# Kernel tuning notes

Hardware: AMD Instinct MI355X
Metric: run time of the kernel (lower is better)

## Reference

```python
import jax, jax.numpy as jnp
import numpy as np

RADIUS = 0.1
MAX_NEIGHBORS = 64


def setup_inputs() -> dict:
    key0 = jax.random.key(0)
    k1, k2 = jax.random.split(key0)
    query = jax.random.uniform(k1, (4, 2048, 3), dtype=jnp.float32)
    key = jax.random.uniform(k2, (4, 8192, 3), dtype=jnp.float32)
    return {"query": query, "key": key}


def reference(query, key):
    # PointNet++-style ball query: for each query point, the indices of the
    # first MAX_NEIGHBORS key points (in key order) with squared distance
    # < RADIUS^2; remaining slots are padded with the first found neighbor
    # index (0 if no neighbor exists, matching zero-initialized CUDA output).
    B, N1, _ = query.shape
    N2 = key.shape[1]
    K = MAX_NEIGHBORS

    # [B, N1, N2] squared pairwise distances
    d2 = jnp.sum((query[:, :, None, :] - key[:, None, :, :]) ** 2, axis=-1)
    within = d2 < jnp.float32(RADIUS) ** 2  # [B, N1, N2] bool

    # slot each valid neighbor lands in (in key-index order)
    pos = jnp.cumsum(within.astype(jnp.int32), axis=-1) - 1  # [B, N1, N2]
    take = within & (pos < K)
    slot = jnp.where(take, pos, K)  # invalid entries routed to dummy slot K

    n2_idx = jnp.broadcast_to(jnp.arange(N2, dtype=jnp.int32), (B, N1, N2))
    b_idx = jnp.arange(B)[:, None, None]
    n1_idx = jnp.arange(N1)[None, :, None]

    out = jnp.full((B, N1, K + 1), -1, dtype=jnp.int32)
    # slots < K are unique per (b, n1); duplicates only at dummy slot K
    out = out.at[b_idx, n1_idx, slot].set(n2_idx)
    out = out[..., :K]  # drop dummy slot

    # pad empty slots with index of first in-radius neighbor (0 if none)
    first = jnp.argmax(within, axis=-1).astype(jnp.int32)  # [B, N1]
    out = jnp.where(out < 0, first[..., None], out)
    return out
```

## Files before the change

kernel.cpp:

```cpp
#include <hip/hip_runtime.h>


constexpr int   K    = 64;
constexpr float R2   = 0.01f;
constexpr int   B    = 4;
constexpr int   N1   = 2048;
constexpr int   N2   = 8192;
constexpr int   GC   = 5;
constexpr int   NCELL = GC * GC * GC;
constexpr float INVCELL = 5.0f;
constexpr int   SUBS_PER_B = 32;
constexpr int   SUBS       = B * SUBS_PER_B;

constexpr size_t SORTED_BYTES = (size_t)B * N2 * 16;
constexpr size_t CS_BYTES     = (size_t)B * (NCELL + 1) * 4;
constexpr size_t WS_NEEDED    = SORTED_BYTES + CS_BYTES;

__device__ __forceinline__ int cell_of(float v) {
    int c = (int)(v * INVCELL);
    return c < 0 ? 0 : (c > GC - 1 ? GC - 1 : c);
}

__global__ __launch_bounds__(256) void build_kernel(
    const float* __restrict__ key,
    int* __restrict__ cell_start,
    float4* __restrict__ sorted)
{
    __shared__ int h_tot[NCELL];
    __shared__ int h_pre[NCELL];
    __shared__ int sbuf[128];
    __shared__ int cursor[NCELL];

    const int k = blockIdx.x;
    const int b = k >> 5;
    const int s = k & 31;
    const int t = threadIdx.x;

    if (t < NCELL) { h_tot[t] = 0; h_pre[t] = 0; }
    __syncthreads();

    const float* kb = key + (size_t)b * N2 * 3;
    float mx = 0.f, my = 0.f, mz = 0.f;
    int mycell = 0;
    for (int i = 0; i < SUBS_PER_B; ++i) {
        const int j = i * 256 + t;
        const float x = kb[j * 3 + 0];
        const float y = kb[j * 3 + 1];
        const float z = kb[j * 3 + 2];
        const int c = (cell_of(x) * GC + cell_of(y)) * GC + cell_of(z);
        atomicAdd(&h_tot[c], 1);
        if (i < s) atomicAdd(&h_pre[c], 1);
        if (i == s) { mx = x; my = y; mz = z; mycell = c; }
    }
    __syncthreads();

    const int total = (t < NCELL) ? h_tot[t] : 0;
    if (t < 128) sbuf[t] = total;
    __syncthreads();
    for (int off = 1; off < 128; off <<= 1) {
        int v = 0;
        if (t < 128 && t >= off) v = sbuf[t - off];
        __syncthreads();
        if (t < 128) sbuf[t] += v;
        __syncthreads();
    }
    if (t < NCELL) {
        const int excl = sbuf[t] - total;
        cursor[t] = excl + h_pre[t];
        if (s == 0) {
            cell_start[b * (NCELL + 1) + t + 1] = sbuf[t];
            if (t == 0) cell_start[b * (NCELL + 1)] = 0;
        }
    }
    __syncthreads();

    const int pos = atomicAdd(&cursor[mycell], 1);
    float4 v;
    v.x = mx; v.y = my; v.z = mz; v.w = __int_as_float(s * 256 + t);
    sorted[(size_t)b * N2 + pos] = v;
}

__global__ __launch_bounds__(256) void ballquery_grid_kernel(
    const float* __restrict__ query,
    const float4* __restrict__ sorted,
    const int* __restrict__ cell_start,
    int* __restrict__ out)
{
    __shared__ unsigned int bm[4 * 256];

    const int lane = threadIdx.x & 63;
    const int wv   = threadIdx.x >> 6;
    const int q    = blockIdx.x * 4 + wv;
    const int b    = q >> 11;

    const float qx = query[q * 3 + 0];
    const float qy = query[q * 3 + 1];
    const float qz = query[q * 3 + 2];

    const float ux = qx * INVCELL, uy = qy * INVCELL, uz = qz * INVCELL;
    const int cx = cell_of(qx), cy = cell_of(qy), cz = cell_of(qz);
    const int nx = (ux - cx < 0.5f) ? cx - 1 : cx + 1;
    const int ny = (uy - cy < 0.5f) ? cy - 1 : cy + 1;
    const int nz = (uz - cz < 0.5f) ? cz - 1 : cz + 1;
    const int xlo = max(0, min(cx, nx)), xhi = min(GC - 1, max(cx, nx));
    const int ylo = max(0, min(cy, ny)), yhi = min(GC - 1, max(cy, ny));
    const int zlo = max(0, min(cz, nz)), zhi = min(GC - 1, max(cz, nz));

    unsigned int* wbm = bm + wv * 256;
    uint4 zz; zz.x = zz.y = zz.z = zz.w = 0u;
    ((uint4*)wbm)[lane] = zz;

    const int*    cs = cell_start + b * (NCELL + 1);
    const float4* sb = sorted + (size_t)b * N2;

    for (int xx = xlo; xx <= xhi; ++xx) {
        for (int yy = ylo; yy <= yhi; ++yy) {
            const int colz = (xx * GC + yy) * GC;
            const int s = cs[colz + zlo];
            const int e = cs[colz + zhi + 1];
            for (int t0 = s; t0 < e; t0 += 64) {
                const int i = t0 + lane;
                const float4 kv = sb[min(i, e - 1)];
                const float dx = kv.x - qx;
                const float dy = kv.y - qy;
                const float dz = kv.z - qz;
                const bool within = (i < e) && (dx * dx + dy * dy + dz * dz < R2);
                if (within) {
                    const int id = __float_as_int(kv.w);
                    atomicOr(&wbm[id >> 5], 1u << (id & 31));
                }
            }
        }
    }

    const uint4 w = ((const uint4*)wbm)[lane];
    const int c = __popc(w.x) + __popc(w.y) + __popc(w.z) + __popc(w.w);

    int x = c;
    #pragma unroll
    for (int off = 1; off < 64; off <<= 1) {
        int y = __shfl_up(x, off);
        if (lane >= off) x += y;
    }
    const int base = x - c;
    const int cnt  = __shfl(x, 63);

    int fs;
    if      (w.x) fs = __builtin_ctz(w.x);
    else if (w.y) fs = 32 + __builtin_ctz(w.y);
    else if (w.z) fs = 64 + __builtin_ctz(w.z);
    else if (w.w) fs = 96 + __builtin_ctz(w.w);
    else          fs = 0;
    int myfirst = c ? (lane << 7) + fs : 0x7fffffff;
    #pragma unroll
    for (int off = 32; off; off >>= 1)
        myfirst = min(myfirst, __shfl_xor(myfirst, off));
    const int firstIdx = (cnt == 0) ? 0 : myfirst;

    int* op = out + q * K;
    int slot = base;
    unsigned int wr[4] = {w.x, w.y, w.z, w.w};
    #pragma unroll
    for (int r = 0; r < 4; ++r) {
        unsigned int m = wr[r];
        const int bb = (lane << 7) + (r << 5);
        while (m) {
            const int bp = __builtin_ctz(m);
            m &= m - 1;
            if (slot < K) op[slot] = bb + bp;
            ++slot;
        }
    }

    const int kpad = cnt < K ? cnt : K;
    const int s2 = kpad + lane;
    if (s2 < K) op[s2] = firstIdx;
}

__global__ __launch_bounds__(256) void ballquery_bruteforce_kernel(
    const float* __restrict__ query, const float* __restrict__ key,
    int* __restrict__ out)
{
    const int lane = threadIdx.x & 63;
    const int q = blockIdx.x * 4 + (threadIdx.x >> 6);
    const int b = q >> 11;
    const float qx = query[q * 3], qy = query[q * 3 + 1], qz = query[q * 3 + 2];
    const float* kb = key + (size_t)b * N2 * 3;
    int* op = out + (size_t)q * K;
    int count = 0, first = 0;
    bool have_first = false;
    const unsigned long long lane_mask_lt = (lane == 0) ? 0ull : (~0ull >> (64 - lane));
    for (int c = 0; c < N2 / 64; ++c) {
        if (count >= K) break;
        const int j = (c << 6) + lane;
        const float* kp = kb + j * 3;
        const float dx = kp[0] - qx, dy = kp[1] - qy, dz = kp[2] - qz;
        const bool within = dx * dx + dy * dy + dz * dz < R2;
        const unsigned long long mask = __ballot(within);
        if (mask) {
            if (!have_first) { first = (c << 6) + __builtin_ctzll(mask); have_first = true; }
            if (within) {
                const int slot = count + __popcll(mask & lane_mask_lt);
                if (slot < K) op[slot] = j;
            }
            count += __popcll(mask);
        }
    }
    const int cnt = count < K ? count : K;
    if (cnt + lane < K) op[cnt + lane] = first;
}

extern "C" void kernel_launch(void* const* d_in, const int* in_sizes, int n_in,
                              void* d_out, int out_size, void* d_ws, size_t ws_size,
                              hipStream_t stream) {
    const float* query = (const float*)d_in[0];
    const float* key   = (const float*)d_in[1];
    int* out = (int*)d_out;

    if (ws_size < WS_NEEDED) {
        ballquery_bruteforce_kernel<<<(B * N1) / 4, 256, 0, stream>>>(query, key, out);
        return;
    }

    float4* sorted     = (float4*)d_ws;
    int*    cell_start = (int*)((char*)d_ws + SORTED_BYTES);

    build_kernel<<<SUBS, 256, 0, stream>>>(key, cell_start, sorted);
    ballquery_grid_kernel<<<(B * N1) / 4, 256, 0, stream>>>(query, sorted, cell_start, out);
}
```

Measured before the change: 76.09 us.

## Build cell grid with one 1024-thread block per batch; pair queries in brute-force

The grid build now runs one 1024-thread block per batch. Each thread holds 8 keys in registers, builds a single histogram and scatters its keys, replacing 32 blocks per batch that each re-read all keys to compute prefix counts. This cuts redundant global reads and atomics but leaves only 4 blocks on the GPU, so the build is less parallel. The brute-force fallback now handles two queries per wave to reuse key loads, and drops the early exit once 64 neighbors are found. That fallback only runs when the workspace is too small.

Result: faster. 72.50 us (-4.7%).

```diff
diff --git a/kernel.cpp b/kernel.cpp
--- a/kernel.cpp
+++ b/kernel.cpp
@@ -9,8 +9,7 @@
 constexpr int   GC   = 5;
 constexpr int   NCELL = GC * GC * GC;
 constexpr float INVCELL = 5.0f;
-constexpr int   SUBS_PER_B = 32;
-constexpr int   SUBS       = B * SUBS_PER_B;
+constexpr int   KPT  = N2 / 1024;
 
 constexpr size_t SORTED_BYTES = (size_t)B * N2 * 16;
 constexpr size_t CS_BYTES     = (size_t)B * (NCELL + 1) * 4;
@@ -21,40 +20,36 @@
     return c < 0 ? 0 : (c > GC - 1 ? GC - 1 : c);
 }
 
-__global__ __launch_bounds__(256) void build_kernel(
+__global__ __launch_bounds__(1024) void build_kernel(
     const float* __restrict__ key,
     int* __restrict__ cell_start,
     float4* __restrict__ sorted)
 {
-    __shared__ int h_tot[NCELL];
-    __shared__ int h_pre[NCELL];
+    __shared__ int h[NCELL];
     __shared__ int sbuf[128];
     __shared__ int cursor[NCELL];
 
-    const int k = blockIdx.x;
-    const int b = k >> 5;
-    const int s = k & 31;
+    const int b = blockIdx.x;
     const int t = threadIdx.x;
 
-    if (t < NCELL) { h_tot[t] = 0; h_pre[t] = 0; }
+    if (t < NCELL) h[t] = 0;
     __syncthreads();
 
     const float* kb = key + (size_t)b * N2 * 3;
-    float mx = 0.f, my = 0.f, mz = 0.f;
-    int mycell = 0;
-    for (int i = 0; i < SUBS_PER_B; ++i) {
-        const int j = i * 256 + t;
-        const float x = kb[j * 3 + 0];
-        const float y = kb[j * 3 + 1];
-        const float z = kb[j * 3 + 2];
-        const int c = (cell_of(x) * GC + cell_of(y)) * GC + cell_of(z);
-        atomicAdd(&h_tot[c], 1);
-        if (i < s) atomicAdd(&h_pre[c], 1);
-        if (i == s) { mx = x; my = y; mz = z; mycell = c; }
-    }
-    __syncthreads();
-
-    const int total = (t < NCELL) ? h_tot[t] : 0;
+    float kx[KPT], ky[KPT], kz[KPT];
+    int   kc[KPT];
+    #pragma unroll
+    for (int i = 0; i < KPT; ++i) {
+        const int j = i * 1024 + t;
+        kx[i] = kb[j * 3 + 0];
+        ky[i] = kb[j * 3 + 1];
+        kz[i] = kb[j * 3 + 2];
+        kc[i] = (cell_of(kx[i]) * GC + cell_of(ky[i])) * GC + cell_of(kz[i]);
+        atomicAdd(&h[kc[i]], 1);
+    }
+    __syncthreads();
+
+    const int total = (t < NCELL) ? h[t] : 0;
     if (t < 128) sbuf[t] = total;
     __syncthreads();
     for (int off = 1; off < 128; off <<= 1) {
@@ -65,19 +60,21 @@
         __syncthreads();
     }
     if (t < NCELL) {
-        const int excl = sbuf[t] - total;
-        cursor[t] = excl + h_pre[t];
-        if (s == 0) {
-            cell_start[b * (NCELL + 1) + t + 1] = sbuf[t];
-            if (t == 0) cell_start[b * (NCELL + 1)] = 0;
-        }
-    }
-    __syncthreads();
-
-    const int pos = atomicAdd(&cursor[mycell], 1);
-    float4 v;
-    v.x = mx; v.y = my; v.z = mz; v.w = __int_as_float(s * 256 + t);
-    sorted[(size_t)b * N2 + pos] = v;
+        cursor[t] = sbuf[t] - total;
+        cell_start[b * (NCELL + 1) + t + 1] = sbuf[t];
+        if (t == 0) cell_start[b * (NCELL + 1)] = 0;
+    }
+    __syncthreads();
+
+    float4* sb = sorted + (size_t)b * N2;
+    #pragma unroll
+    for (int i = 0; i < KPT; ++i) {
+        const int pos = atomicAdd(&cursor[kc[i]], 1);
+        float4 v;
+        v.x = kx[i]; v.y = ky[i]; v.z = kz[i];
+        v.w = __int_as_float(i * 1024 + t);
+        sb[pos] = v;
+    }
 }
 
 __global__ __launch_bounds__(256) void ballquery_grid_kernel(
@@ -177,37 +174,66 @@
     if (s2 < K) op[s2] = firstIdx;
 }
 
-__global__ __launch_bounds__(256) void ballquery_bruteforce_kernel(
+__global__ __launch_bounds__(256) void bq_brute2_kernel(
     const float* __restrict__ query, const float* __restrict__ key,
     int* __restrict__ out)
 {
     const int lane = threadIdx.x & 63;
-    const int q = blockIdx.x * 4 + (threadIdx.x >> 6);
-    const int b = q >> 11;
-    const float qx = query[q * 3], qy = query[q * 3 + 1], qz = query[q * 3 + 2];
+    const int w    = blockIdx.x * 4 + (threadIdx.x >> 6);
+    const int q0   = w * 2;
+    const int q1   = q0 + 1;
+    const int b    = q0 >> 11;
+
+    const float qx0 = query[q0 * 3 + 0], qy0 = query[q0 * 3 + 1], qz0 = query[q0 * 3 + 2];
+    const float qx1 = query[q1 * 3 + 0], qy1 = query[q1 * 3 + 1], qz1 = query[q1 * 3 + 2];
+
     const float* kb = key + (size_t)b * N2 * 3;
-    int* op = out + (size_t)q * K;
-    int count = 0, first = 0;
-    bool have_first = false;
-    const unsigned long long lane_mask_lt = (lane == 0) ? 0ull : (~0ull >> (64 - lane));
+    const unsigned long long below = (lane == 0) ? 0ull : (~0ull >> (64 - lane));
+
+    int cnt0 = 0, cnt1 = 0, f0 = -1, f1 = -1;
+    int* op0 = out + (size_t)q0 * K;
+    int* op1 = out + (size_t)q1 * K;
+
+    #pragma unroll 4
     for (int c = 0; c < N2 / 64; ++c) {
-        if (count >= K) break;
         const int j = (c << 6) + lane;
-        const float* kp = kb + j * 3;
-        const float dx = kp[0] - qx, dy = kp[1] - qy, dz = kp[2] - qz;
-        const bool within = dx * dx + dy * dy + dz * dz < R2;
-        const unsigned long long mask = __ballot(within);
-        if (mask) {
-            if (!have_first) { first = (c << 6) + __builtin_ctzll(mask); have_first = true; }
-            if (within) {
-                const int slot = count + __popcll(mask & lane_mask_lt);
-                if (slot < K) op[slot] = j;
+        const float x = kb[j * 3 + 0];
+        const float y = kb[j * 3 + 1];
+        const float z = kb[j * 3 + 2];
+        {
+            const float dx = x - qx0, dy = y - qy0, dz = z - qz0;
+            const bool within = dx * dx + dy * dy + dz * dz < R2;
+            const unsigned long long m = __ballot(within);
+            if (m) {
+                if (f0 < 0) f0 = (c << 6) + __builtin_ctzll(m);
+                if (within) {
+                    const int slot = cnt0 + __popcll(m & below);
+                    if (slot < K) op0[slot] = j;
+                }
+                cnt0 += __popcll(m);
             }
-            count += __popcll(mask);
-        }
-    }
-    const int cnt = count < K ? count : K;
-    if (cnt + lane < K) op[cnt + lane] = first;
+        }
+        {
+            const float dx = x - qx1, dy = y - qy1, dz = z - qz1;
+            const bool within = dx * dx + dy * dy + dz * dz < R2;
+            const unsigned long long m = __ballot(within);
+            if (m) {
+                if (f1 < 0) f1 = (c << 6) + __builtin_ctzll(m);
+                if (within) {
+                    const int slot = cnt1 + __popcll(m & below);
+                    if (slot < K) op1[slot] = j;
+                }
+                cnt1 += __popcll(m);
+            }
+        }
+    }
+
+    const int first0 = (f0 < 0) ? 0 : f0;
+    const int first1 = (f1 < 0) ? 0 : f1;
+    const int c0 = cnt0 < K ? cnt0 : K;
+    const int c1 = cnt1 < K ? cnt1 : K;
+    if (c0 + lane < K) op0[c0 + lane] = first0;
+    if (c1 + lane < K) op1[c1 + lane] = first1;
 }
 
 extern "C" void kernel_launch(void* const* d_in, const int* in_sizes, int n_in,
@@ -218,13 +244,13 @@
     int* out = (int*)d_out;
 
     if (ws_size < WS_NEEDED) {
-        ballquery_bruteforce_kernel<<<(B * N1) / 4, 256, 0, stream>>>(query, key, out);
+        bq_brute2_kernel<<<(B * N1) / 8, 256, 0, stream>>>(query, key, out);
         return;
     }
 
     float4* sorted     = (float4*)d_ws;
     int*    cell_start = (int*)((char*)d_ws + SORTED_BYTES);
 
-    build_kernel<<<SUBS, 256, 0, stream>>>(key, cell_start, sorted);
+    build_kernel<<<B, 1024, 0, stream>>>(key, cell_start, sorted);
     ballquery_grid_kernel<<<(B * N1) / 4, 256, 0, stream>>>(query, sorted, cell_start, out);
 }
```
